# Kernel optimization log

Measured on AMD Instinct MI355X. Metric: run time of the kernel, lower is better.

The kernel has to match this reference:

```python
import jax, jax.numpy as jnp
import numpy as np

N_RUNS, T, N_AGENTS, SENSING = 128, 2048, 16, 7
HIDDEN, OUT = 22, 2


def setup_inputs() -> dict:
    key = jax.random.key(0)
    k_runs, k_comm, k_w1, k_b1, k_w2, k_b2 = jax.random.split(key, 6)
    runs = jax.random.normal(k_runs, (N_RUNS, T, N_AGENTS, SENSING), dtype=jnp.float32)
    # init_comm: zero boundary pads, uniform(0,1) interior, one vector per run
    comm_init = jax.random.uniform(k_comm, (N_RUNS, N_AGENTS + 2), dtype=jnp.float32)
    comm_init = comm_init.at[:, 0].set(0.0).at[:, -1].set(0.0)
    W1 = jax.random.normal(k_w1, (HIDDEN, SENSING + 2), dtype=jnp.float32) * (1.0 / np.sqrt(SENSING + 2))
    b1 = jax.random.normal(k_b1, (HIDDEN,), dtype=jnp.float32) * 0.01
    W2 = jax.random.normal(k_w2, (OUT, HIDDEN), dtype=jnp.float32) * (1.0 / np.sqrt(HIDDEN))
    b2 = jax.random.normal(k_b2, (OUT,), dtype=jnp.float32) * 0.01
    return {"runs": runs, "comm_init": comm_init, "W1": W1, "b1": b1, "W2": W2, "b2": b2}


def reference(runs, comm_init, W1, b1, W2, b2):
    # Sync.sequential: agents processed in index order; agent i reads comm[i]
    # (freshly written by agent i-1) and comm[i+2], then writes comm[i+1].
    n_agents = runs.shape[2]

    def agent_step(carry, i):
        comm, xs_t = carry  # comm: [N+2], xs_t: [N, 7]
        inp = jnp.concatenate([xs_t[i], jnp.stack([comm[i], comm[i + 2]])])  # [9]
        h = jax.nn.relu(W1 @ inp + b1)
        out = W2 @ h + b2  # [2]: (control, new_comm)
        comm = comm.at[i + 1].set(out[1])
        return (comm, xs_t), out[0]

    def time_step(comm, xs_t):
        (comm, _), controls = jax.lax.scan(agent_step, (comm, xs_t), jnp.arange(n_agents))
        return comm, controls  # controls: [N]

    def run_fn(run, comm0):
        # comm persists across timesteps within a run
        _, controls = jax.lax.scan(time_step, comm0, run)
        return controls  # [T, N]

    return jax.vmap(run_fn)(runs, comm_init)  # [n_runs, T, N]
```

## Files before the change

kernel.cpp:

```cpp
#include <hip/hip_runtime.h>

#define NRUNS  128
#define TSTEPS 2048
#define NAG    16
#define SENS   7
#define HID    22
#define HP     24
#define HPRE_BYTES ((size_t)NRUNS * TSTEPS * NAG * HP * 2)

typedef float float2v __attribute__((ext_vector_type(2)));
typedef _Float16 half2v __attribute__((ext_vector_type(2)));

template<int CTRL>
__device__ __forceinline__ float dpp_mov(float v) {
    return __int_as_float(__builtin_amdgcn_update_dpp(
        0, __float_as_int(v), CTRL, 0xf, 0xf, true));
}

__device__ __forceinline__ float grp_sum_r(float v) {
    v += dpp_mov<0x128>(v);
    unsigned u = __float_as_uint(v);
    auto r = __builtin_amdgcn_permlane32_swap(u, u, false, false);
    return __uint_as_float(r[0]) + __uint_as_float(r[1]);
}

__global__ void __launch_bounds__(256) hpre_kernel(
    const float* __restrict__ runs, const float* __restrict__ W1,
    const float* __restrict__ b1, _Float16* __restrict__ hpre)
{
    const int tid = blockIdx.x * 256 + threadIdx.x;
    const int s8  = tid & 7;
    const int rb  = tid >> 3;
    float w[3][SENS], bb[3];
#pragma unroll
    for (int u = 0; u < 3; ++u) {
        int j = s8 * 3 + u; bool valid = j < HID; int jj = valid ? j : 0;
        float m = valid ? 1.f : 0.f;
#pragma unroll
        for (int k = 0; k < SENS; ++k) w[u][k] = m * W1[jj * 9 + k];
        bb[u] = m * b1[jj];
    }
#pragma unroll 1
    for (int q = 0; q < 64; ++q) {
        long r = (long)rb + (long)q * 65536;
        const float* x = runs + r * SENS;
        float x0=x[0],x1=x[1],x2=x[2],x3=x[3],x4=x[4],x5=x[5],x6=x[6];
        _Float16* hw = hpre + r * HP + s8 * 3;
#pragma unroll
        for (int u = 0; u < 3; ++u) {
            float a = bb[u];
            a = fmaf(w[u][0], x0, a); a = fmaf(w[u][1], x1, a);
            a = fmaf(w[u][2], x2, a); a = fmaf(w[u][3], x3, a);
            a = fmaf(w[u][4], x4, a); a = fmaf(w[u][5], x5, a);
            a = fmaf(w[u][6], x6, a);
            hw[u] = (_Float16)a;
        }
    }
}

struct HBlk { half2v h[2][6]; };

__global__ void __launch_bounds__(64, 1) comm_net_kernel(
    const half2v* __restrict__ hpre2,
    const float* __restrict__ W1,
    const float* __restrict__ W2,
    const float* __restrict__ b2,
    const float* __restrict__ comm_init,
    float* __restrict__ out)
{
    const int run  = blockIdx.x;
    const int lane = threadIdx.x & 63;
    const int g    = lane & 7;
    const int sub2 = ((lane >> 3) & 1) | ((lane >> 4) & 2);
    const bool g0  = (g == 0);
    const bool g7  = (g == 7);

    float wA[6], wAm[6], wB[6], wBm[6], w20[6], w21[6];
#pragma unroll
    for (int v = 0; v < 6; ++v) {
        int j = sub2 * 6 + v; bool valid = j < HID; int jj = valid ? j : 0;
        float m = valid ? 1.f : 0.f;
        float wa = m * W1[jj * 9 + 7];
        float wb = m * W1[jj * 9 + 8];
        wA[v] = wa; wAm[v] = g0 ? 0.f : wa;
        wB[v] = wb; wBm[v] = g7 ? 0.f : wb;
        w20[v] = m * W2[jj];
        w21[v] = m * W2[HID + jj];
    }
    const float b20s = (sub2 == 0) ? b2[0] : 0.f;
    const float b21s = (sub2 == 0) ? b2[1] : 0.f;

    const float* ci = comm_init + run * (NAG + 2);
    float prevV = ci[2 * g + 2];
    const float initV_e = ci[2 * g + 1];
    const float initV_o = ci[2 * g + 2];

    const half2v* hp2 = hpre2 + (long)run * (TSTEPS * NAG * HP / 2);
    float*        po  = out   + (size_t)run * TSTEPS * NAG;

    auto substep_even = [&](const float (&h)[6], float& o0out) {
        float cL = dpp_mov<0x111>(prevV);
        float a[6];
#pragma unroll
        for (int v = 0; v < 6; ++v)
            a[v] = fmaxf(fmaf(wAm[v], cL, fmaf(wB[v], prevV, h[v])), 0.f);
        float q0a = fmaf(w20[1], a[1], fmaf(w20[0], a[0], b20s));
        float q0b = fmaf(w20[3], a[3], w20[2] * a[2]);
        float q0c = fmaf(w20[5], a[5], w20[4] * a[4]);
        float q1a = fmaf(w21[1], a[1], fmaf(w21[0], a[0], b21s));
        float q1b = fmaf(w21[3], a[3], w21[2] * a[2]);
        float q1c = fmaf(w21[5], a[5], w21[4] * a[4]);
        prevV = grp_sum_r((q1a + q1b) + q1c);
        o0out = grp_sum_r((q0a + q0b) + q0c);
    };
    auto substep_odd = [&](const float (&h)[6], float& o0out) {
        float cR = dpp_mov<0x101>(prevV);
        float a[6];
#pragma unroll
        for (int v = 0; v < 6; ++v)
            a[v] = fmaxf(fmaf(wBm[v], cR, fmaf(wA[v], prevV, h[v])), 0.f);
        float q0a = fmaf(w20[1], a[1], fmaf(w20[0], a[0], b20s));
        float q0b = fmaf(w20[3], a[3], w20[2] * a[2]);
        float q0c = fmaf(w20[5], a[5], w20[4] * a[4]);
        float q1a = fmaf(w21[1], a[1], fmaf(w21[0], a[0], b21s));
        float q1b = fmaf(w21[3], a[3], w21[2] * a[2]);
        float q1c = fmaf(w21[5], a[5], w21[4] * a[4]);
        prevV = grp_sum_r((q1a + q1b) + q1c);
        o0out = grp_sum_r((q0a + q0b) + q0c);
    };

    auto ramp_pair = [&](int s) {
        int t  = (s >> 1) - g;
        int tc = t < 0 ? 0 : (t > TSTEPS - 1 ? TSTEPS - 1 : t);
        long db = (long)tc * 192 + (2 * g) * 12 + sub2 * 3;
        float he[6], ho[6];
#pragma unroll
        for (int k = 0; k < 3; ++k) {
            half2v e = hp2[db + k], o = hp2[db + 12 + k];
            he[2*k] = (float)e.x; he[2*k+1] = (float)e.y;
            ho[2*k] = (float)o.x; ho[2*k+1] = (float)o.y;
        }
        bool inr = (t >= 0) && (t < TSTEPS);
        float o0;
        substep_even(he, o0);
        if (inr) po[(size_t)t * NAG + 2 * g] = o0;
        prevV = (t < 0) ? initV_e : prevV;
        substep_odd(ho, o0);
        if (inr) po[(size_t)t * NAG + 2 * g + 1] = o0;
        prevV = (t < 0) ? initV_o : prevV;
    };

#pragma unroll 1
    for (int s = 0; s <= 14; s += 2) ramp_pair(s);

    const long db0 = ((long)(8 - g) * NAG + 2 * g) * 12 + sub2 * 3;
    float* oe = po + (size_t)(8 - g) * NAG + 2 * g;

    auto load_blk = [&](HBlk& H, long db) {
#pragma unroll
        for (int j = 0; j < 2; ++j)
#pragma unroll
            for (int k = 0; k < 3; ++k) {
                H.h[j][k]     = hp2[db + j * 192 + k];
                H.h[j][3 + k] = hp2[db + j * 192 + 12 + k];
            }
    };
    auto process_blk = [&](const HBlk& H) {
#pragma unroll
        for (int j = 0; j < 2; ++j) {
            float he[6], ho[6];
#pragma unroll
            for (int k = 0; k < 3; ++k) {
                he[2*k] = (float)H.h[j][k].x;     he[2*k+1] = (float)H.h[j][k].y;
                ho[2*k] = (float)H.h[j][3+k].x;   ho[2*k+1] = (float)H.h[j][3+k].y;
            }
            float o0;
            substep_even(he, o0); oe[0] = o0;
            substep_odd (ho, o0); oe[1] = o0;
            oe += NAG;
        }
    };

    HBlk HA, HB, HC, HD;
    load_blk(HA, db0);
    load_blk(HB, db0 + 384);
    load_blk(HC, db0 + 768);
    load_blk(HD, db0 + 1152);
#pragma unroll 1
    for (int bm = 0; bm < 1016; bm += 4) {
        process_blk(HA); load_blk(HA, db0 + (long)(bm + 4) * 384);
        process_blk(HB); load_blk(HB, db0 + (long)(bm + 5) * 384);
        process_blk(HC); load_blk(HC, db0 + (long)(bm + 6) * 384);
        process_blk(HD); load_blk(HD, db0 + (long)(bm + 7) * 384);
    }
    process_blk(HA); process_blk(HB); process_blk(HC); process_blk(HD);

#pragma unroll 1
    for (int s = 2 * TSTEPS; s <= 2 * TSTEPS + 12; s += 2) ramp_pair(s);
}

__device__ __forceinline__ float grp_reduce_fb(float v) {
    v += dpp_mov<0xB1>(v);
    v += dpp_mov<0x4E>(v);
    v += dpp_mov<0x141>(v);
    return v;
}
__device__ __forceinline__ float bperm_fb(int byteaddr, float v) {
    return __int_as_float(__builtin_amdgcn_ds_bpermute(byteaddr, __float_as_int(v)));
}
struct RawBlk { float2v v[4][7]; };
struct XpBlk  { float e[4][3]; float o[4][3]; };

__global__ void __launch_bounds__(64, 1) comm_net_fb(
    const float* __restrict__ runs, const float* __restrict__ comm_init,
    const float* __restrict__ W1, const float* __restrict__ b1,
    const float* __restrict__ W2, const float* __restrict__ b2,
    float* __restrict__ out)
{
    const int run  = blockIdx.x;
    const int lane = threadIdx.x & 63;
    const int g    = lane >> 3;
    const int sub  = lane & 7;
    const bool g0  = (g == 0);
    const bool g7  = (g == 7);
    float w1x[3][SENS], wA[3], wB[3], b1v[3], w20[3], w21[3];
#pragma unroll
    for (int u = 0; u < 3; ++u) {
        int j = sub * 3 + u; bool valid = (j < HID); int jj = valid ? j : 0;
        float m = valid ? 1.0f : 0.0f;
#pragma unroll
        for (int k = 0; k < SENS; ++k) w1x[u][k] = m * W1[jj * 9 + k];
        wA[u] = m * W1[jj * 9 + 7]; wB[u] = m * W1[jj * 9 + 8];
        b1v[u] = m * b1[jj]; w20[u] = m * W2[jj]; w21[u] = m * W2[HID + jj];
    }
    const float b20 = b2[0], b21 = b2[1];
    const int addr_even = ((lane - 8) & 63) * 4;
    const int addr_odd  = ((lane + 8) & 63) * 4;
    const float* ci = comm_init + run * (NAG + 2);
    float prevV = ci[2 * g + 2];
    const float initV_e = ci[2 * g + 1];
    const float initV_o = ci[2 * g + 2];
    const float* pr = runs + (size_t)run * TSTEPS * NAG * SENS;
    float*       po = out  + (size_t)run * TSTEPS * NAG;
    auto xpart_pair = [&](const float2v (&r)[7], float (&ae)[3], float (&ao)[3]) {
#pragma unroll
        for (int u = 0; u < 3; ++u) {
            float e = b1v[u];
            e = fmaf(w1x[u][0], r[0].x, e); e = fmaf(w1x[u][1], r[0].y, e);
            e = fmaf(w1x[u][2], r[1].x, e); e = fmaf(w1x[u][3], r[1].y, e);
            e = fmaf(w1x[u][4], r[2].x, e); e = fmaf(w1x[u][5], r[2].y, e);
            e = fmaf(w1x[u][6], r[3].x, e);
            ae[u] = e;
            float o = b1v[u];
            o = fmaf(w1x[u][0], r[3].y, o); o = fmaf(w1x[u][1], r[4].x, o);
            o = fmaf(w1x[u][2], r[4].y, o); o = fmaf(w1x[u][3], r[5].x, o);
            o = fmaf(w1x[u][4], r[5].y, o); o = fmaf(w1x[u][5], r[6].x, o);
            o = fmaf(w1x[u][6], r[6].y, o);
            ao[u] = o;
        }
    };
    auto substep_even = [&](float x0, float x1, float x2, float& o0out) {
        float cross = bperm_fb(addr_even, prevV);
        float cL = g0 ? 0.f : cross;
        float a0 = fmaxf(fmaf(wA[0], cL, fmaf(wB[0], prevV, x0)), 0.f);
        float a1 = fmaxf(fmaf(wA[1], cL, fmaf(wB[1], prevV, x1)), 0.f);
        float a2 = fmaxf(fmaf(wA[2], cL, fmaf(wB[2], prevV, x2)), 0.f);
        float p0 = w20[0]*a0; p0 = fmaf(w20[1],a1,p0); p0 = fmaf(w20[2],a2,p0);
        float p1 = w21[0]*a0; p1 = fmaf(w21[1],a1,p1); p1 = fmaf(w21[2],a2,p1);
        o0out = grp_reduce_fb(p0) + b20;
        prevV = grp_reduce_fb(p1) + b21;
    };
    auto substep_odd = [&](float x0, float x1, float x2, float& o0out) {
        float cross = bperm_fb(addr_odd, prevV);
        float cR = g7 ? 0.f : cross;
        float a0 = fmaxf(fmaf(wB[0], cR, fmaf(wA[0], prevV, x0)), 0.f);
        float a1 = fmaxf(fmaf(wB[1], cR, fmaf(wA[1], prevV, x1)), 0.f);
        float a2 = fmaxf(fmaf(wB[2], cR, fmaf(wA[2], prevV, x2)), 0.f);
        float p0 = w20[0]*a0; p0 = fmaf(w20[1],a1,p0); p0 = fmaf(w20[2],a2,p0);
        float p1 = w21[0]*a0; p1 = fmaf(w21[1],a1,p1); p1 = fmaf(w21[2],a2,p1);
        o0out = grp_reduce_fb(p0) + b20;
        prevV = grp_reduce_fb(p1) + b21;
    };
    auto ramp_pair = [&](int s) {
        int t  = (s >> 1) - g;
        int tc = t < 0 ? 0 : (t > TSTEPS - 1 ? TSTEPS - 1 : t);
        const float2v* xp = (const float2v*)(pr + ((size_t)tc * NAG + 2 * g) * SENS);
        float2v r[7];
#pragma unroll
        for (int k = 0; k < 7; ++k) r[k] = xp[k];
        float ae[3], ao[3];
        xpart_pair(r, ae, ao);
        bool inr = (t >= 0) && (t < TSTEPS);
        float o0;
        substep_even(ae[0], ae[1], ae[2], o0);
        if (inr) po[(size_t)t * NAG + 2 * g] = o0;
        prevV = (t < 0) ? initV_e : prevV;
        substep_odd(ao[0], ao[1], ao[2], o0);
        if (inr) po[(size_t)t * NAG + 2 * g + 1] = o0;
        prevV = (t < 0) ? initV_o : prevV;
    };
#pragma unroll 1
    for (int s = 0; s <= 14; s += 2) ramp_pair(s);
    const float2v* xv = (const float2v*)(pr + ((size_t)(8 - g) * NAG + 2 * g) * SENS);
    float* oe = po + (size_t)(8 - g) * NAG + 2 * g;
    RawBlk RA, RB; XpBlk P0, P1;
    auto load_blk = [&](RawBlk& R, const float2v* p) {
#pragma unroll
        for (int j = 0; j < 4; ++j)
#pragma unroll
            for (int k = 0; k < 7; ++k) R.v[j][k] = p[j * 56 + k];
    };
    auto xpart_blk = [&](XpBlk& P, const RawBlk& R) {
#pragma unroll
        for (int j = 0; j < 4; ++j) xpart_pair(R.v[j], P.e[j], P.o[j]);
    };
    auto process_blk = [&](const XpBlk& P) {
#pragma unroll
        for (int j = 0; j < 4; ++j) {
            float o0;
            substep_even(P.e[j][0], P.e[j][1], P.e[j][2], o0); oe[0] = o0;
            substep_odd (P.o[j][0], P.o[j][1], P.o[j][2], o0); oe[1] = o0;
            oe += NAG;
        }
    };
    load_blk(RA, xv); load_blk(RB, xv + 224);
    xpart_blk(P0, RA); load_blk(RA, xv + 2 * 224);
#pragma unroll 1
    for (int bm = 0; bm < 506; bm += 2) {
        xpart_blk(P1, RB); load_blk(RB, xv + (size_t)(bm + 3) * 224);
        process_blk(P0);
        xpart_blk(P0, RA); load_blk(RA, xv + (size_t)(bm + 4) * 224);
        process_blk(P1);
    }
    xpart_blk(P1, RB); load_blk(RB, xv + (size_t)509 * 224);
    process_blk(P0);
    xpart_blk(P0, RA); process_blk(P1);
    xpart_blk(P1, RB); process_blk(P0); process_blk(P1);
#pragma unroll 1
    for (int s = 2 * TSTEPS; s <= 2 * TSTEPS + 12; s += 2) ramp_pair(s);
}

extern "C" void kernel_launch(void* const* d_in, const int* in_sizes, int n_in,
                              void* d_out, int out_size, void* d_ws, size_t ws_size,
                              hipStream_t stream) {
    const float* runs      = (const float*)d_in[0];
    const float* comm_init = (const float*)d_in[1];
    const float* W1        = (const float*)d_in[2];
    const float* b1        = (const float*)d_in[3];
    const float* W2        = (const float*)d_in[4];
    const float* b2        = (const float*)d_in[5];
    float* out = (float*)d_out;

    if (ws_size >= HPRE_BYTES) {
        _Float16* hpre = (_Float16*)d_ws;
        hipLaunchKernelGGL(hpre_kernel, dim3(2048), dim3(256), 0, stream,
                           runs, W1, b1, hpre);
        hipLaunchKernelGGL(comm_net_kernel, dim3(NRUNS), dim3(64), 0, stream,
                           (const half2v*)hpre, W1, W2, b2, comm_init, out);
    } else {
        hipLaunchKernelGGL(comm_net_fb, dim3(NRUNS), dim3(64), 0, stream,
                           runs, comm_init, W1, b1, W2, b2, out);
    }
}
```

Measured before the change: 514.0 us.

## Defer control-output reduction to a finalize kernel off the serial chain

The recurrent kernel no longer reduces the control output across lanes at each agent substep. Each lane writes its partial sum into the workspace, reusing the already-consumed pre-activation rows, and a new finalize kernel sums the partials and adds the bias. This removes one cross-lane reduction per substep from the latency-bound sequential chain, at the cost of an extra kernel launch and additional global memory traffic. The pre-activation kernel is also regrouped to compute six hidden units per thread and write them as packed 12-byte stores, and the fp16-to-fp32 conversion now happens inside the substep.

Result: faster. 472.3 us (-8.1%).

```diff
diff --git a/kernel.cpp b/kernel.cpp
--- a/kernel.cpp
+++ b/kernel.cpp
@@ -6,10 +6,12 @@
 #define SENS   7
 #define HID    22
 #define HP     24
-#define HPRE_BYTES ((size_t)NRUNS * TSTEPS * NAG * HP * 2)
+#define NROWS  ((long)NRUNS * TSTEPS * NAG)
+#define HPRE_BYTES ((size_t)NROWS * HP * 2)
 
 typedef float float2v __attribute__((ext_vector_type(2)));
 typedef _Float16 half2v __attribute__((ext_vector_type(2)));
+typedef unsigned int uint3v __attribute__((ext_vector_type(3)));
 
 template<int CTRL>
 __device__ __forceinline__ float dpp_mov(float v) {
@@ -26,52 +28,60 @@
 
 __global__ void __launch_bounds__(256) hpre_kernel(
     const float* __restrict__ runs, const float* __restrict__ W1,
-    const float* __restrict__ b1, _Float16* __restrict__ hpre)
+    const float* __restrict__ b1, char* __restrict__ hpre)
 {
     const int tid = blockIdx.x * 256 + threadIdx.x;
-    const int s8  = tid & 7;
-    const int rb  = tid >> 3;
-    float w[3][SENS], bb[3];
-#pragma unroll
-    for (int u = 0; u < 3; ++u) {
-        int j = s8 * 3 + u; bool valid = j < HID; int jj = valid ? j : 0;
+    const int q   = tid & 3;
+    const int rr  = tid >> 2;
+    float w[6][SENS], bb[6];
+#pragma unroll
+    for (int u = 0; u < 6; ++u) {
+        int j = q * 6 + u; bool valid = j < HID; int jj = valid ? j : 0;
         float m = valid ? 1.f : 0.f;
 #pragma unroll
         for (int k = 0; k < SENS; ++k) w[u][k] = m * W1[jj * 9 + k];
         bb[u] = m * b1[jj];
     }
 #pragma unroll 1
-    for (int q = 0; q < 64; ++q) {
-        long r = (long)rb + (long)q * 65536;
+    for (int it = 0; it < 16; ++it) {
+        long r = (long)rr + (long)it * 262144;
         const float* x = runs + r * SENS;
         float x0=x[0],x1=x[1],x2=x[2],x3=x[3],x4=x[4],x5=x[5],x6=x[6];
-        _Float16* hw = hpre + r * HP + s8 * 3;
-#pragma unroll
-        for (int u = 0; u < 3; ++u) {
+        float h[6];
+#pragma unroll
+        for (int u = 0; u < 6; ++u) {
             float a = bb[u];
             a = fmaf(w[u][0], x0, a); a = fmaf(w[u][1], x1, a);
             a = fmaf(w[u][2], x2, a); a = fmaf(w[u][3], x3, a);
             a = fmaf(w[u][4], x4, a); a = fmaf(w[u][5], x5, a);
             a = fmaf(w[u][6], x6, a);
-            hw[u] = (_Float16)a;
-        }
-    }
-}
-
-struct HBlk { half2v h[2][6]; };
+            h[u] = a;
+        }
+        uint3v wv;
+#pragma unroll
+        for (int k = 0; k < 3; ++k) {
+            half2v p; p.x = (_Float16)h[2*k]; p.y = (_Float16)h[2*k+1];
+            wv[k] = __builtin_bit_cast(unsigned int, p);
+        }
+        *(uint3v*)(hpre + r * 48 + q * 12) = wv;
+    }
+}
+
+struct HBlk { unsigned int e[2][3], o[2][3]; };
 
 __global__ void __launch_bounds__(64, 1) comm_net_kernel(
-    const half2v* __restrict__ hpre2,
+    const unsigned int* __restrict__ hpu,
+    char* __restrict__ scratch,
     const float* __restrict__ W1,
     const float* __restrict__ W2,
     const float* __restrict__ b2,
-    const float* __restrict__ comm_init,
-    float* __restrict__ out)
+    const float* __restrict__ comm_init)
 {
     const int run  = blockIdx.x;
     const int lane = threadIdx.x & 63;
     const int g    = lane & 7;
     const int sub2 = ((lane >> 3) & 1) | ((lane >> 4) & 2);
+    const int s4   = (lane >> 3) * 4;
     const bool g0  = (g == 0);
     const bool g7  = (g == 7);
 
@@ -87,7 +97,6 @@
         w20[v] = m * W2[jj];
         w21[v] = m * W2[HID + jj];
     }
-    const float b20s = (sub2 == 0) ? b2[0] : 0.f;
     const float b21s = (sub2 == 0) ? b2[1] : 0.f;
 
     const float* ci = comm_init + run * (NAG + 2);
@@ -95,58 +104,55 @@
     const float initV_e = ci[2 * g + 1];
     const float initV_o = ci[2 * g + 2];
 
-    const half2v* hp2 = hpre2 + (long)run * (TSTEPS * NAG * HP / 2);
-    float*        po  = out   + (size_t)run * TSTEPS * NAG;
-
-    auto substep_even = [&](const float (&h)[6], float& o0out) {
+    const unsigned int* hp = hpu + (long)run * (TSTEPS * NAG * 12);
+    char* scr = scratch + (long)run * (TSTEPS * NAG * 48);
+
+    auto sub_e = [&](const unsigned int (&hd)[3]) -> float {
         float cL = dpp_mov<0x111>(prevV);
         float a[6];
 #pragma unroll
-        for (int v = 0; v < 6; ++v)
-            a[v] = fmaxf(fmaf(wAm[v], cL, fmaf(wB[v], prevV, h[v])), 0.f);
-        float q0a = fmaf(w20[1], a[1], fmaf(w20[0], a[0], b20s));
-        float q0b = fmaf(w20[3], a[3], w20[2] * a[2]);
-        float q0c = fmaf(w20[5], a[5], w20[4] * a[4]);
-        float q1a = fmaf(w21[1], a[1], fmaf(w21[0], a[0], b21s));
-        float q1b = fmaf(w21[3], a[3], w21[2] * a[2]);
-        float q1c = fmaf(w21[5], a[5], w21[4] * a[4]);
-        prevV = grp_sum_r((q1a + q1b) + q1c);
-        o0out = grp_sum_r((q0a + q0b) + q0c);
-    };
-    auto substep_odd = [&](const float (&h)[6], float& o0out) {
+        for (int k = 0; k < 3; ++k) {
+            half2v h2 = __builtin_bit_cast(half2v, hd[k]);
+            a[2*k]   = fmaxf(fmaf(wAm[2*k],   cL, fmaf(wB[2*k],   prevV, (float)h2.x)), 0.f);
+            a[2*k+1] = fmaxf(fmaf(wAm[2*k+1], cL, fmaf(wB[2*k+1], prevV, (float)h2.y)), 0.f);
+        }
+        float q1x = fmaf(w21[0],a[0], fmaf(w21[2],a[2], fmaf(w21[4],a[4], b21s)));
+        float q1y = fmaf(w21[1],a[1], fmaf(w21[3],a[3], w21[5]*a[5]));
+        prevV = grp_sum_r(q1x + q1y);
+        float q0x = fmaf(w20[0],a[0], fmaf(w20[2],a[2], w20[4]*a[4]));
+        float q0y = fmaf(w20[1],a[1], fmaf(w20[3],a[3], w20[5]*a[5]));
+        return q0x + q0y;
+    };
+    auto sub_o = [&](const unsigned int (&hd)[3]) -> float {
         float cR = dpp_mov<0x101>(prevV);
         float a[6];
 #pragma unroll
-        for (int v = 0; v < 6; ++v)
-            a[v] = fmaxf(fmaf(wBm[v], cR, fmaf(wA[v], prevV, h[v])), 0.f);
-        float q0a = fmaf(w20[1], a[1], fmaf(w20[0], a[0], b20s));
-        float q0b = fmaf(w20[3], a[3], w20[2] * a[2]);
-        float q0c = fmaf(w20[5], a[5], w20[4] * a[4]);
-        float q1a = fmaf(w21[1], a[1], fmaf(w21[0], a[0], b21s));
-        float q1b = fmaf(w21[3], a[3], w21[2] * a[2]);
-        float q1c = fmaf(w21[5], a[5], w21[4] * a[4]);
-        prevV = grp_sum_r((q1a + q1b) + q1c);
-        o0out = grp_sum_r((q0a + q0b) + q0c);
+        for (int k = 0; k < 3; ++k) {
+            half2v h2 = __builtin_bit_cast(half2v, hd[k]);
+            a[2*k]   = fmaxf(fmaf(wBm[2*k],   cR, fmaf(wA[2*k],   prevV, (float)h2.x)), 0.f);
+            a[2*k+1] = fmaxf(fmaf(wBm[2*k+1], cR, fmaf(wA[2*k+1], prevV, (float)h2.y)), 0.f);
+        }
+        float q1x = fmaf(w21[0],a[0], fmaf(w21[2],a[2], fmaf(w21[4],a[4], b21s)));
+        float q1y = fmaf(w21[1],a[1], fmaf(w21[3],a[3], w21[5]*a[5]));
+        prevV = grp_sum_r(q1x + q1y);
+        float q0x = fmaf(w20[0],a[0], fmaf(w20[2],a[2], w20[4]*a[4]));
+        float q0y = fmaf(w20[1],a[1], fmaf(w20[3],a[3], w20[5]*a[5]));
+        return q0x + q0y;
     };
 
     auto ramp_pair = [&](int s) {
         int t  = (s >> 1) - g;
         int tc = t < 0 ? 0 : (t > TSTEPS - 1 ? TSTEPS - 1 : t);
         long db = (long)tc * 192 + (2 * g) * 12 + sub2 * 3;
-        float he[6], ho[6];
-#pragma unroll
-        for (int k = 0; k < 3; ++k) {
-            half2v e = hp2[db + k], o = hp2[db + 12 + k];
-            he[2*k] = (float)e.x; he[2*k+1] = (float)e.y;
-            ho[2*k] = (float)o.x; ho[2*k+1] = (float)o.y;
-        }
+        unsigned int he[3], ho[3];
+#pragma unroll
+        for (int k = 0; k < 3; ++k) { he[k] = hp[db + k]; ho[k] = hp[db + 12 + k]; }
         bool inr = (t >= 0) && (t < TSTEPS);
-        float o0;
-        substep_even(he, o0);
-        if (inr) po[(size_t)t * NAG + 2 * g] = o0;
+        float q0 = sub_e(he);
+        if (inr) *(float*)(scr + (long)(t * NAG + 2 * g) * 48 + s4) = q0;
         prevV = (t < 0) ? initV_e : prevV;
-        substep_odd(ho, o0);
-        if (inr) po[(size_t)t * NAG + 2 * g + 1] = o0;
+        q0 = sub_o(ho);
+        if (inr) *(float*)(scr + (long)(t * NAG + 2 * g + 1) * 48 + s4) = q0;
         prevV = (t < 0) ? initV_o : prevV;
     };
 
@@ -154,30 +160,25 @@
     for (int s = 0; s <= 14; s += 2) ramp_pair(s);
 
     const long db0 = ((long)(8 - g) * NAG + 2 * g) * 12 + sub2 * 3;
-    float* oe = po + (size_t)(8 - g) * NAG + 2 * g;
+    char* qp = scr + (long)((8 - g) * NAG + 2 * g) * 48 + s4;
 
     auto load_blk = [&](HBlk& H, long db) {
 #pragma unroll
         for (int j = 0; j < 2; ++j)
 #pragma unroll
             for (int k = 0; k < 3; ++k) {
-                H.h[j][k]     = hp2[db + j * 192 + k];
-                H.h[j][3 + k] = hp2[db + j * 192 + 12 + k];
+                H.e[j][k] = hp[db + j * 192 + k];
+                H.o[j][k] = hp[db + j * 192 + 12 + k];
             }
     };
     auto process_blk = [&](const HBlk& H) {
 #pragma unroll
         for (int j = 0; j < 2; ++j) {
-            float he[6], ho[6];
-#pragma unroll
-            for (int k = 0; k < 3; ++k) {
-                he[2*k] = (float)H.h[j][k].x;     he[2*k+1] = (float)H.h[j][k].y;
-                ho[2*k] = (float)H.h[j][3+k].x;   ho[2*k+1] = (float)H.h[j][3+k].y;
-            }
-            float o0;
-            substep_even(he, o0); oe[0] = o0;
-            substep_odd (ho, o0); oe[1] = o0;
-            oe += NAG;
+            float q0 = sub_e(H.e[j]);
+            *(float*)qp = q0;
+            q0 = sub_o(H.o[j]);
+            *(float*)(qp + 48) = q0;
+            qp += 16 * 48;
         }
     };
 
@@ -197,6 +198,17 @@
 
 #pragma unroll 1
     for (int s = 2 * TSTEPS; s <= 2 * TSTEPS + 12; s += 2) ramp_pair(s);
+}
+
+__global__ void __launch_bounds__(256) finalize_kernel(
+    const char* __restrict__ scratch, const float* __restrict__ b2,
+    float* __restrict__ out)
+{
+    long r = (long)blockIdx.x * 256 + threadIdx.x;
+    const float* p = (const float*)(scratch + r * 48);
+    float2v ab = *(const float2v*)p;
+    float2v cd = *(const float2v*)(p + 4);
+    out[r] = b2[0] + ((ab.x + ab.y) + (cd.x + cd.y));
 }
 
 __device__ __forceinline__ float grp_reduce_fb(float v) {
@@ -352,11 +364,13 @@
     float* out = (float*)d_out;
 
     if (ws_size >= HPRE_BYTES) {
-        _Float16* hpre = (_Float16*)d_ws;
-        hipLaunchKernelGGL(hpre_kernel, dim3(2048), dim3(256), 0, stream,
+        char* hpre = (char*)d_ws;
+        hipLaunchKernelGGL(hpre_kernel, dim3(4096), dim3(256), 0, stream,
                            runs, W1, b1, hpre);
         hipLaunchKernelGGL(comm_net_kernel, dim3(NRUNS), dim3(64), 0, stream,
-                           (const half2v*)hpre, W1, W2, b2, comm_init, out);
+                           (const unsigned int*)hpre, hpre, W1, W2, b2, comm_init);
+        hipLaunchKernelGGL(finalize_kernel, dim3(16384), dim3(256), 0, stream,
+                           (const char*)hpre, b2, out);
     } else {
         hipLaunchKernelGGL(comm_net_fb, dim3(NRUNS), dim3(64), 0, stream,
                            runs, comm_init, W1, b1, W2, b2, out);
```
